# Kernel tuning notes

Measured on AMD Instinct MI355X. Metric: run time of the kernel, lower is better.

## Reference

```python
import jax, jax.numpy as jnp
import numpy as np

N_NODES = 50000
N_EDGES = 800000
D = 64
B = 64
HL = 128  # lstm hidden
OUT = 32


def setup_inputs() -> dict:
    key = jax.random.key(0)
    ks = jax.random.split(key, 16)
    s = 0.05
    return {
        "x": jax.random.normal(ks[0], (N_NODES, D), jnp.float32),
        "edge_index": jax.random.randint(ks[1], (2, N_EDGES), 0, N_NODES),
        "batch": jnp.sort(jax.random.randint(ks[2], (N_NODES,), 0, B)),
        "w1": jax.random.normal(ks[3], (D, D), jnp.float32) * s,
        "b1": jnp.zeros((D,), jnp.float32),
        "w2": jax.random.normal(ks[4], (D, D), jnp.float32) * s,
        "b2": jnp.zeros((D,), jnp.float32),
        "w3": jax.random.normal(ks[5], (D, D), jnp.float32) * s,
        "b3": jnp.zeros((D,), jnp.float32),
        "w4": jax.random.normal(ks[6], (D, D), jnp.float32) * s,
        "b4": jnp.zeros((D,), jnp.float32),
        "w_ih": jax.random.normal(ks[7], (4 * HL, D), jnp.float32) * s,
        "w_hh": jax.random.normal(ks[8], (4 * HL, HL), jnp.float32) * s,
        "b_ih": jnp.zeros((4 * HL,), jnp.float32),
        "b_hh": jnp.zeros((4 * HL,), jnp.float32),
        "fc_w": jax.random.normal(ks[9], (OUT, HL), jnp.float32) * s,
        "fc_b": jnp.zeros((OUT,), jnp.float32),
        "h0": jax.random.normal(ks[10], (1, B, HL), jnp.float32),
        "c0": jax.random.normal(ks[11], (1, B, HL), jnp.float32),
    }


def _gin(x, edge_index, wA, bA, wB, bB):
    # GINConv with eps=0: MLP(x + sum_{j->i} x_j); scatter-add over edges
    agg = jax.ops.segment_sum(x[edge_index[0]], edge_index[1], num_segments=N_NODES)
    h = x + agg
    h = jax.nn.relu(h @ wA.T + bA)
    return h @ wB.T + bB


def reference(x, edge_index, batch, w1, b1, w2, b2, w3, b3, w4, b4,
              w_ih, w_hh, b_ih, b_hh, fc_w, fc_b, h0, c0):
    h = jax.nn.relu(_gin(x, edge_index, w1, b1, w2, b2))  # dropout = identity (eval)
    h = jax.nn.relu(_gin(h, edge_index, w3, b3, w4, b4))
    # global_mean_pool over graphs
    sums = jax.ops.segment_sum(h, batch, num_segments=B)              # [B, D]
    cnts = jax.ops.segment_sum(jnp.ones((N_NODES,), h.dtype), batch, num_segments=B)
    pooled = sums / jnp.maximum(cnts, 1.0)[:, None]
    # single-step LSTM (PyTorch gate order: i, f, g, o)
    gates = pooled @ w_ih.T + b_ih + h0[0] @ w_hh.T + b_hh            # [B, 4H]
    i, f, g, o = jnp.split(gates, 4, axis=-1)
    c1 = jax.nn.sigmoid(f) * c0[0] + jax.nn.sigmoid(i) * jnp.tanh(g)
    h1 = jax.nn.sigmoid(o) * jnp.tanh(c1)
    logits = h1 @ fc_w.T + fc_b
    probs = jax.nn.softmax(logits, axis=1)
    return probs, h1[None], c1[None]
```

## Files before the change

### kernel.cpp

```cpp
#include <hip/hip_runtime.h>
#include <hip/hip_bf16.h>

#define N_NODES 50000
#define N_EDGES 800000
#define D 64
#define B 64
#define HL 128
#define OUT 32

#define CAP 64
#define STP 72
#define ZROW N_NODES

#define BINS 196
#define EPB 2048
#define LCAP 48
#define BCAP 4608

#define AB 391
#define CB 3125
#define MB 782

typedef __attribute__((ext_vector_type(8))) short          short8;
typedef __attribute__((ext_vector_type(8))) unsigned short ushort8_t;
typedef __attribute__((ext_vector_type(4))) float          floatx4;

__device__ __forceinline__ unsigned short f2bf(float f)
{
    unsigned u = __float_as_uint(f);
    u = (u + 0x7FFFu + ((u >> 16) & 1u)) >> 16;
    return (unsigned short)u;
}
__device__ __forceinline__ float bf2f(unsigned short s)
{
    return __uint_as_float(((unsigned)s) << 16);
}
__device__ __forceinline__ float bfLO(unsigned u) { return __uint_as_float(u << 16); }
__device__ __forceinline__ float bfHI(unsigned u) { return __uint_as_float(u & 0xffff0000u); }

__global__ __launch_bounds__(256) void fused_pro_kernel(
    const int*   __restrict__ ei,
    int*         __restrict__ bincnt,
    unsigned*    __restrict__ binbuf,
    const float* __restrict__ x, unsigned short* __restrict__ xb,
    const float* __restrict__ w1, const float* __restrict__ w2,
    const float* __restrict__ w3, const float* __restrict__ w4,
    unsigned short* __restrict__ wb,
    unsigned short* __restrict__ h1,
    float*       __restrict__ psum)
{
    __shared__ int      lcnt[BINS];
    __shared__ int      gbase[BINS];
    __shared__ unsigned lbuf[BINS * LCAP];

    int t = threadIdx.x;

    if (blockIdx.x < AB) {
        if (t < BINS) lcnt[t] = 0;
        __syncthreads();

        int base = blockIdx.x * EPB;
#pragma unroll
        for (int i = 0; i < EPB / 256; ++i) {
            int e = base + i * 256 + t;
            if (e < N_EDGES) {
                int s = ei[e];
                int d = ei[N_EDGES + e];
                int bin = d >> 8;
                unsigned pk = (unsigned)s | ((unsigned)(d & 255) << 16);
                int p = atomicAdd(&lcnt[bin], 1);
                if (p < LCAP) {
                    lbuf[bin * LCAP + p] = pk;
                } else {
                    int q = atomicAdd(&bincnt[bin], 1);
                    if (q < BCAP) binbuf[bin * BCAP + q] = pk;
                }
            }
        }
        __syncthreads();

        if (t < BINS) {
            int m = lcnt[t]; m = (m < LCAP) ? m : LCAP;
            gbase[t] = (m > 0) ? atomicAdd(&bincnt[t], m) : 0;
        }
        __syncthreads();

        int wv = t >> 6, lane = t & 63;
        for (int b = wv; b < BINS; b += 4) {
            int m = lcnt[b]; m = (m < LCAP) ? m : LCAP;
            int gb = gbase[b];
            for (int j = lane; j < m; j += 64)
                if (gb + j < BCAP) binbuf[b * BCAP + gb + j] = lbuf[b * LCAP + j];
        }
    } else if (blockIdx.x < AB + CB) {
        int cb = blockIdx.x - AB;
        int i = cb * 256 + t;
        const float4 v = reinterpret_cast<const float4*>(x)[i];
        ushort4 o;
        o.x = f2bf(v.x); o.y = f2bf(v.y); o.z = f2bf(v.z); o.w = f2bf(v.w);
        reinterpret_cast<ushort4*>(xb)[i] = o;

        if (cb < 64) {
            int j = cb * 256 + t;
            int m = j >> 12, off = j & 4095;
            const float* src = (m == 0) ? w1 : (m == 1) ? w2 : (m == 2) ? w3 : w4;
            wb[j] = f2bf(src[off]);
        }
    } else {
        if (t < D) {
            xb[(size_t)ZROW * D + t] = 0;
            h1[(size_t)ZROW * D + t] = 0;
        }
#pragma unroll
        for (int k = 0; k < 16; ++k)
            psum[t * 16 + k] = 0.0f;
    }
}

__device__ __forceinline__ void build_bucket64(
    const int*      __restrict__ bincnt,
    const unsigned* __restrict__ binbuf,
    unsigned short* lbkt,
    int*            lc,
    int bn0, int t)
{
    {
        ushort8_t fill = {ZROW, ZROW, ZROW, ZROW, ZROW, ZROW, ZROW, ZROW};
        reinterpret_cast<ushort8_t*>(lbkt)[t]       = fill;
        reinterpret_cast<ushort8_t*>(lbkt)[t + 256] = fill;
    }
    if (t < 64) lc[t] = 0;
    __syncthreads();

    const int bin = bn0 >> 8;
    const int q   = (bn0 >> 6) & 3;
    int m = bincnt[bin]; m = (m < BCAP) ? m : BCAP;
    const unsigned* src = binbuf + bin * BCAP;
    for (int j = t; j < m; j += 256) {
        unsigned pk = src[j];
        int dlow = (pk >> 16) & 255;
        if ((dlow >> 6) == q) {
            int r = dlow & 63;
            int p = atomicAdd(&lc[r], 1);
            if (p < CAP) lbkt[r * CAP + p] = (unsigned short)(pk & 0xFFFFu);
        }
    }
    __syncthreads();
}

__device__ __forceinline__ void gather16_lds(
    const unsigned short* __restrict__ feat,
    const unsigned short* lbkt,
    const int*            lc,
    unsigned short*       stw,
    int bn0, int wv, int lane)
{
    const int g = lane >> 4;
    const int c = lane & 15;

#pragma unroll
    for (int b = 0; b < 4; ++b) {
        const int rloc = wv * 16 + b * 4 + g;
        const int node = bn0 + rloc;
        int deg = lc[rloc];
        deg = (deg < CAP) ? deg : CAP;
        int m = (deg + 7) >> 3;
        {
            int t1 = __shfl_xor(m, 16); m = (t1 > m) ? t1 : m;
            int t2 = __shfl_xor(m, 32); m = (t2 > m) ? t2 : m;
        }

        const unsigned short* bkt = lbkt + rloc * CAP;

        uint2 u = *reinterpret_cast<const uint2*>(feat + (size_t)node * D + 4 * c);
        float a0 = bfLO(u.x), a1 = bfHI(u.x);
        float a2 = bfLO(u.y), a3 = bfHI(u.y);

        ushort8_t idx = *reinterpret_cast<const ushort8_t*>(bkt);
        for (int r = 0; r < m; ++r) {
            ushort8_t nxt = *reinterpret_cast<const ushort8_t*>(bkt + (r + 1) * 8);
#pragma unroll
            for (int j = 0; j < 8; ++j) {
                uint2 v = *reinterpret_cast<const uint2*>(
                    feat + (size_t)idx[j] * D + 4 * c);
                a0 += bfLO(v.x); a1 += bfHI(v.x);
                a2 += bfLO(v.y); a3 += bfHI(v.y);
            }
            idx = nxt;
        }

        uint2 o;
        o.x = (unsigned)f2bf(a0) | ((unsigned)f2bf(a1) << 16);
        o.y = (unsigned)f2bf(a2) | ((unsigned)f2bf(a3) << 16);
        *reinterpret_cast<uint2*>(stw + (b * 4 + g) * STP + 4 * c) = o;
    }
}

__global__ __launch_bounds__(256) void gmlp_kernel(
    const unsigned short* __restrict__ feat,
    const int*            __restrict__ bincnt,
    const unsigned*       __restrict__ binbuf,
    const unsigned short* __restrict__ wAb,
    const float*          __restrict__ bA,
    const unsigned short* __restrict__ wBb,
    const float*          __restrict__ bB,
    unsigned short*       __restrict__ outp)
{
    __shared__ int lc[64];
    __shared__ __align__(16) unsigned short lbkt[64 * CAP + 16];
    __shared__ __align__(16) unsigned short st[4][16 * STP];

    const int t    = threadIdx.x;
    const int wv   = t >> 6;
    const int lane = t & 63;
    const int quad = lane >> 4;
    const int col  = lane & 15;

    const int bn0 = blockIdx.x * 64;
    const int n0  = bn0 + wv * 16;

    build_bucket64(bincnt, binbuf, lbkt, lc, bn0, t);

    if (n0 >= N_NODES) return;

    float bAl[4], bBl[4];
#pragma unroll
    for (int tt = 0; tt < 4; ++tt) {
        bAl[tt] = bA[tt * 16 + col];
        bBl[tt] = bB[tt * 16 + col];
    }

    short8 WA[4][2], WB[4][2];
#pragma unroll
    for (int tt = 0; tt < 4; ++tt)
#pragma unroll
        for (int k = 0; k < 2; ++k) {
            WA[tt][k] = *reinterpret_cast<const short8*>(
                wAb + (tt * 16 + col) * D + k * 32 + quad * 8);
            WB[tt][k] = *reinterpret_cast<const short8*>(
                wBb + (tt * 16 + col) * D + k * 32 + quad * 8);
        }

    unsigned short* stw = &st[wv][0];

    gather16_lds(feat, lbkt, lc, stw, bn0, wv, lane);

    short8 A0 = *reinterpret_cast<const short8*>(stw + col * STP + 0 * 32 + quad * 8);
    short8 A1 = *reinterpret_cast<const short8*>(stw + col * STP + 1 * 32 + quad * 8);

#pragma unroll
    for (int tt = 0; tt < 4; ++tt) {
        floatx4 c = {0.0f, 0.0f, 0.0f, 0.0f};
        c = __builtin_amdgcn_mfma_f32_16x16x32_bf16(A0, WA[tt][0], c, 0, 0, 0);
        c = __builtin_amdgcn_mfma_f32_16x16x32_bf16(A1, WA[tt][1], c, 0, 0, 0);
#pragma unroll
        for (int r = 0; r < 4; ++r) {
            float v = fmaxf(c[r] + bAl[tt], 0.0f);
            stw[(quad * 4 + r) * STP + tt * 16 + col] = f2bf(v);
        }
    }

    short8 T0 = *reinterpret_cast<const short8*>(stw + col * STP + 0 * 32 + quad * 8);
    short8 T1 = *reinterpret_cast<const short8*>(stw + col * STP + 1 * 32 + quad * 8);

#pragma unroll
    for (int tt = 0; tt < 4; ++tt) {
        floatx4 c = {0.0f, 0.0f, 0.0f, 0.0f};
        c = __builtin_amdgcn_mfma_f32_16x16x32_bf16(T0, WB[tt][0], c, 0, 0, 0);
        c = __builtin_amdgcn_mfma_f32_16x16x32_bf16(T1, WB[tt][1], c, 0, 0, 0);
#pragma unroll
        for (int r = 0; r < 4; ++r) {
            float v = fmaxf(c[r] + bBl[tt], 0.0f);
            outp[(size_t)(n0 + quad * 4 + r) * D + tt * 16 + col] = f2bf(v);
        }
    }
}

__global__ __launch_bounds__(256) void g2mlp_pool_kernel(
    const unsigned short* __restrict__ feat,
    const int*            __restrict__ bincnt,
    const unsigned*       __restrict__ binbuf,
    const unsigned short* __restrict__ wAb,
    const float*          __restrict__ bA,
    const unsigned short* __restrict__ wBb,
    const float*          __restrict__ bB,
    const int*            __restrict__ batch,
    float*                __restrict__ psum)
{
    __shared__ int lc[64];
    __shared__ __align__(16) unsigned short lbkt[64 * CAP + 16];
    __shared__ __align__(16) unsigned short st[4][16 * STP];
    __shared__ float pt[64][D + 1];
    __shared__ int   sbatch[64];

    const int t    = threadIdx.x;
    const int wv   = t >> 6;
    const int lane = t & 63;
    const int quad = lane >> 4;
    const int col  = lane & 15;

    const int bn0 = blockIdx.x * 64;
    const int n0  = bn0 + wv * 16;
    const bool active = (n0 < N_NODES);

    if (t < 64) {
        int n = bn0 + t;
        sbatch[t] = (n < N_NODES) ? batch[n] : -1;
    }

    build_bucket64(bincnt, binbuf, lbkt, lc, bn0, t);

    if (active) {
        float bAl[4], bBl[4];
#pragma unroll
        for (int tt = 0; tt < 4; ++tt) {
            bAl[tt] = bA[tt * 16 + col];
            bBl[tt] = bB[tt * 16 + col];
        }

        short8 WA[4][2], WB[4][2];
#pragma unroll
        for (int tt = 0; tt < 4; ++tt)
#pragma unroll
            for (int k = 0; k < 2; ++k) {
                WA[tt][k] = *reinterpret_cast<const short8*>(
                    wAb + (tt * 16 + col) * D + k * 32 + quad * 8);
                WB[tt][k] = *reinterpret_cast<const short8*>(
                    wBb + (tt * 16 + col) * D + k * 32 + quad * 8);
            }

        unsigned short* stw = &st[wv][0];

        gather16_lds(feat, lbkt, lc, stw, bn0, wv, lane);

        short8 A0 = *reinterpret_cast<const short8*>(stw + col * STP + 0 * 32 + quad * 8);
        short8 A1 = *reinterpret_cast<const short8*>(stw + col * STP + 1 * 32 + quad * 8);

#pragma unroll
        for (int tt = 0; tt < 4; ++tt) {
            floatx4 c = {0.0f, 0.0f, 0.0f, 0.0f};
            c = __builtin_amdgcn_mfma_f32_16x16x32_bf16(A0, WA[tt][0], c, 0, 0, 0);
            c = __builtin_amdgcn_mfma_f32_16x16x32_bf16(A1, WA[tt][1], c, 0, 0, 0);
#pragma unroll
            for (int r = 0; r < 4; ++r) {
                float v = fmaxf(c[r] + bAl[tt], 0.0f);
                stw[(quad * 4 + r) * STP + tt * 16 + col] = f2bf(v);
            }
        }

        short8 T0 = *reinterpret_cast<const short8*>(stw + col * STP + 0 * 32 + quad * 8);
        short8 T1 = *reinterpret_cast<const short8*>(stw + col * STP + 1 * 32 + quad * 8);

#pragma unroll
        for (int tt = 0; tt < 4; ++tt) {
            floatx4 c = {0.0f, 0.0f, 0.0f, 0.0f};
            c = __builtin_amdgcn_mfma_f32_16x16x32_bf16(T0, WB[tt][0], c, 0, 0, 0);
            c = __builtin_amdgcn_mfma_f32_16x16x32_bf16(T1, WB[tt][1], c, 0, 0, 0);
#pragma unroll
            for (int r = 0; r < 4; ++r) {
                float v = fmaxf(c[r] + bBl[tt], 0.0f);
                pt[wv * 16 + quad * 4 + r][tt * 16 + col] = v;
            }
        }
    } else {
        for (int c2 = 0; c2 < 4; ++c2)
#pragma unroll
            for (int r = 0; r < 4; ++r)
                pt[wv * 16 + quad * 4 + r][c2 * 16 + col] = 0.0f;
    }
    __syncthreads();

    int q = t >> 6;
    int d = t & 63;
    float acc = 0.0f;
    int curg = sbatch[q * 16];
#pragma unroll
    for (int r = 0; r < 16; ++r) {
        int row = q * 16 + r;
        int g2 = sbatch[row];
        float v = pt[row][d];
        if (g2 != curg) {
            if (curg >= 0) atomicAdd(&psum[curg * D + d], acc);
            acc = 0.0f;
            curg = g2;
        }
        acc += v;
    }
    if (curg >= 0) atomicAdd(&psum[curg * D + d], acc);
}

__device__ __forceinline__ int lower_bound_dev(const int* a, int n, int v)
{
    int lo = 0, hi = n;
    while (lo < hi) {
        int m = (lo + hi) >> 1;
        if (a[m] < v) lo = m + 1; else hi = m;
    }
    return lo;
}

__device__ __forceinline__ float sigmoidf_(float x) { return 1.0f / (1.0f + expf(-x)); }

__global__ __launch_bounds__(512) void head_kernel(
    const float* __restrict__ psum,
    const int*   __restrict__ batch,
    const float* __restrict__ w_ih,
    const float* __restrict__ w_hh,
    const float* __restrict__ b_ih,
    const float* __restrict__ b_hh,
    const float* __restrict__ fc_w,
    const float* __restrict__ fc_b,
    const float* __restrict__ h0,
    const float* __restrict__ c0,
    float*       __restrict__ out_probs,
    float*       __restrict__ out_h1,
    float*       __restrict__ out_c1)
{
    int b = blockIdx.x;
    int j = threadIdx.x;

    __shared__ float sp[D];
    __shared__ float sh[HL];
    __shared__ float gates[4 * HL];
    __shared__ float sh1[HL];
    __shared__ float slog[OUT];

    if (j < D) {
        int start = lower_bound_dev(batch, N_NODES, b);
        int end   = lower_bound_dev(batch, N_NODES, b + 1);
        sp[j] = psum[b * D + j] / fmaxf((float)(end - start), 1.0f);
    } else if (j < D + HL) {
        sh[j - D] = h0[b * HL + (j - D)];
    }
    __syncthreads();

    {
        float acc = b_ih[j] + b_hh[j];
#pragma unroll
        for (int k = 0; k < D; ++k)  acc = fmaf(sp[k], w_ih[j * D + k], acc);
#pragma unroll
        for (int k = 0; k < HL; ++k) acc = fmaf(sh[k], w_hh[j * HL + k], acc);
        gates[j] = acc;
    }
    __syncthreads();

    if (j < HL) {
        float ig = gates[j];
        float fg = gates[HL + j];
        float gg = gates[2 * HL + j];
        float og = gates[3 * HL + j];
        float c  = sigmoidf_(fg) * c0[b * HL + j] + sigmoidf_(ig) * tanhf(gg);
        float hv = sigmoidf_(og) * tanhf(c);
        out_c1[b * HL + j] = c;
        out_h1[b * HL + j] = hv;
        sh1[j] = hv;
    }
    __syncthreads();

    if (j < OUT) {
        float a = fc_b[j];
#pragma unroll
        for (int k = 0; k < HL; ++k) a = fmaf(sh1[k], fc_w[j * HL + k], a);
        slog[j] = a;
    }
    __syncthreads();

    if (j < OUT) {
        float m = -1e30f;
#pragma unroll
        for (int k = 0; k < OUT; ++k) m = fmaxf(m, slog[k]);
        float s = 0.0f;
#pragma unroll
        for (int k = 0; k < OUT; ++k) s += expf(slog[k] - m);
        out_probs[b * OUT + j] = expf(slog[j] - m) / s;
    }
}

extern "C" void kernel_launch(void* const* d_in, const int* in_sizes, int n_in,
                              void* d_out, int out_size, void* d_ws, size_t ws_size,
                              hipStream_t stream)
{
    const float* x     = (const float*)d_in[0];
    const int*   ei    = (const int*)  d_in[1];
    const int*   batch = (const int*)  d_in[2];
    const float* w1    = (const float*)d_in[3];
    const float* b1    = (const float*)d_in[4];
    const float* w2    = (const float*)d_in[5];
    const float* b2    = (const float*)d_in[6];
    const float* w3    = (const float*)d_in[7];
    const float* b3    = (const float*)d_in[8];
    const float* w4    = (const float*)d_in[9];
    const float* b4    = (const float*)d_in[10];
    const float* w_ih  = (const float*)d_in[11];
    const float* w_hh  = (const float*)d_in[12];
    const float* b_ih  = (const float*)d_in[13];
    const float* b_hh  = (const float*)d_in[14];
    const float* fc_w  = (const float*)d_in[15];
    const float* fc_b  = (const float*)d_in[16];
    const float* h0    = (const float*)d_in[17];
    const float* c0    = (const float*)d_in[18];

    const size_t NR = (size_t)N_NODES + 16;
    int* bincnt = (int*)d_ws;
    unsigned* binbuf = (unsigned*)(bincnt + 256);
    unsigned short* xb = (unsigned short*)(binbuf + (size_t)BINS * BCAP);
    unsigned short* h1 = xb + NR * D;
    unsigned short* wb = h1 + NR * D;
    float* psum = (float*)(wb + 4 * D * D);

    float* out_probs = (float*)d_out;
    float* out_h1    = out_probs + B * OUT;
    float* out_c1    = out_h1 + B * HL;

    hipMemsetAsync(bincnt, 0, 256 * sizeof(int), stream);
    fused_pro_kernel<<<AB + CB + 1, 256, 0, stream>>>(
        ei, bincnt, binbuf, x, xb, w1, w2, w3, w4, wb, h1, psum);

    gmlp_kernel<<<MB, 256, 0, stream>>>(xb, bincnt, binbuf,
                                        wb, b1, wb + 4096, b2, h1);

    g2mlp_pool_kernel<<<MB, 256, 0, stream>>>(h1, bincnt, binbuf,
                                              wb + 8192, b3, wb + 12288, b4,
                                              batch, psum);

    head_kernel<<<B, 512, 0, stream>>>(psum, batch, w_ih, w_hh, b_ih, b_hh,
                                       fc_w, fc_b, h0, c0,
                                       out_probs, out_h1, out_c1);
}
```

Baseline: 199.0 us.

## Batch neighbor gathers across rows, double edges per bin block, fuse pool counts

The neighbor gather now walks all four rows of a wave together. It loads 32 feature vectors per step, which raises memory-level parallelism, at the cost of a shared trip count based on the largest degree and more registers. The edge binning blocks now handle twice as many edges each, so there are fewer blocks and more edges land in each block's local buffer. Per-graph node counts are gathered with atomics in the pooling kernel, replacing the binary searches over the batch array in the head kernel.

```diff
diff --git a/kernel.cpp b/kernel.cpp
--- a/kernel.cpp
+++ b/kernel.cpp
@@ -13,11 +13,11 @@
 #define ZROW N_NODES
 
 #define BINS 196
-#define EPB 2048
+#define EPB 4096
 #define LCAP 48
 #define BCAP 4608
 
-#define AB 391
+#define AB 196
 #define CB 3125
 #define MB 782
 
@@ -31,14 +31,10 @@
     u = (u + 0x7FFFu + ((u >> 16) & 1u)) >> 16;
     return (unsigned short)u;
 }
-__device__ __forceinline__ float bf2f(unsigned short s)
-{
-    return __uint_as_float(((unsigned)s) << 16);
-}
 __device__ __forceinline__ float bfLO(unsigned u) { return __uint_as_float(u << 16); }
 __device__ __forceinline__ float bfHI(unsigned u) { return __uint_as_float(u & 0xffff0000u); }
 
-__global__ __launch_bounds__(256) void fused_pro_kernel(
+__global__ __launch_bounds__(256) void pro_kernel(
     const int*   __restrict__ ei,
     int*         __restrict__ bincnt,
     unsigned*    __restrict__ binbuf,
@@ -47,7 +43,8 @@
     const float* __restrict__ w3, const float* __restrict__ w4,
     unsigned short* __restrict__ wb,
     unsigned short* __restrict__ h1,
-    float*       __restrict__ psum)
+    float*       __restrict__ psum,
+    float*       __restrict__ cnts)
 {
     __shared__ int      lcnt[BINS];
     __shared__ int      gbase[BINS];
@@ -60,7 +57,7 @@
         __syncthreads();
 
         int base = blockIdx.x * EPB;
-#pragma unroll
+#pragma unroll 8
         for (int i = 0; i < EPB / 256; ++i) {
             int e = base + i * 256 + t;
             if (e < N_EDGES) {
@@ -114,6 +111,7 @@
 #pragma unroll
         for (int k = 0; k < 16; ++k)
             psum[t * 16 + k] = 0.0f;
+        if (t < B) cnts[t] = 0.0f;
     }
 }
 
@@ -148,7 +146,7 @@
     __syncthreads();
 }
 
-__device__ __forceinline__ void gather16_lds(
+__device__ __forceinline__ void gather16_bf16(
     const unsigned short* __restrict__ feat,
     const unsigned short* lbkt,
     const int*            lc,
@@ -158,40 +156,57 @@
     const int g = lane >> 4;
     const int c = lane & 15;
 
+    int dmax = 0;
 #pragma unroll
     for (int b = 0; b < 4; ++b) {
-        const int rloc = wv * 16 + b * 4 + g;
-        const int node = bn0 + rloc;
-        int deg = lc[rloc];
-        deg = (deg < CAP) ? deg : CAP;
-        int m = (deg + 7) >> 3;
-        {
-            int t1 = __shfl_xor(m, 16); m = (t1 > m) ? t1 : m;
-            int t2 = __shfl_xor(m, 32); m = (t2 > m) ? t2 : m;
-        }
-
-        const unsigned short* bkt = lbkt + rloc * CAP;
-
+        int d = lc[wv * 16 + b * 4 + g];
+        d = (d < CAP) ? d : CAP;
+        dmax = (d > dmax) ? d : dmax;
+    }
+    int m = (dmax + 7) >> 3;
+    {
+        int t1 = __shfl_xor(m, 16); m = (t1 > m) ? t1 : m;
+        int t2 = __shfl_xor(m, 32); m = (t2 > m) ? t2 : m;
+    }
+
+    float a[4][4];
+#pragma unroll
+    for (int b = 0; b < 4; ++b) {
+        const int node = bn0 + wv * 16 + b * 4 + g;
         uint2 u = *reinterpret_cast<const uint2*>(feat + (size_t)node * D + 4 * c);
-        float a0 = bfLO(u.x), a1 = bfHI(u.x);
-        float a2 = bfLO(u.y), a3 = bfHI(u.y);
-
-        ushort8_t idx = *reinterpret_cast<const ushort8_t*>(bkt);
-        for (int r = 0; r < m; ++r) {
-            ushort8_t nxt = *reinterpret_cast<const ushort8_t*>(bkt + (r + 1) * 8);
+        a[b][0] = bfLO(u.x); a[b][1] = bfHI(u.x);
+        a[b][2] = bfLO(u.y); a[b][3] = bfHI(u.y);
+    }
+
+    for (int r = 0; r < m; ++r) {
+        ushort8_t idx[4];
+#pragma unroll
+        for (int b = 0; b < 4; ++b)
+            idx[b] = *reinterpret_cast<const ushort8_t*>(
+                lbkt + (wv * 16 + b * 4 + g) * CAP + r * 8);
+
+        uint2 v[4][8];
+#pragma unroll
+        for (int b = 0; b < 4; ++b)
+#pragma unroll
+            for (int j = 0; j < 8; ++j)
+                v[b][j] = *reinterpret_cast<const uint2*>(
+                    feat + (size_t)idx[b][j] * D + 4 * c);
+
+#pragma unroll
+        for (int b = 0; b < 4; ++b)
 #pragma unroll
             for (int j = 0; j < 8; ++j) {
-                uint2 v = *reinterpret_cast<const uint2*>(
-                    feat + (size_t)idx[j] * D + 4 * c);
-                a0 += bfLO(v.x); a1 += bfHI(v.x);
-                a2 += bfLO(v.y); a3 += bfHI(v.y);
+                a[b][0] += bfLO(v[b][j].x); a[b][1] += bfHI(v[b][j].x);
+                a[b][2] += bfLO(v[b][j].y); a[b][3] += bfHI(v[b][j].y);
             }
-            idx = nxt;
-        }
-
+    }
+
+#pragma unroll
+    for (int b = 0; b < 4; ++b) {
         uint2 o;
-        o.x = (unsigned)f2bf(a0) | ((unsigned)f2bf(a1) << 16);
-        o.y = (unsigned)f2bf(a2) | ((unsigned)f2bf(a3) << 16);
+        o.x = (unsigned)f2bf(a[b][0]) | ((unsigned)f2bf(a[b][1]) << 16);
+        o.y = (unsigned)f2bf(a[b][2]) | ((unsigned)f2bf(a[b][3]) << 16);
         *reinterpret_cast<uint2*>(stw + (b * 4 + g) * STP + 4 * c) = o;
     }
 }
@@ -243,7 +258,7 @@
 
     unsigned short* stw = &st[wv][0];
 
-    gather16_lds(feat, lbkt, lc, stw, bn0, wv, lane);
+    gather16_bf16(feat, lbkt, lc, stw, bn0, wv, lane);
 
     short8 A0 = *reinterpret_cast<const short8*>(stw + col * STP + 0 * 32 + quad * 8);
     short8 A1 = *reinterpret_cast<const short8*>(stw + col * STP + 1 * 32 + quad * 8);
@@ -285,7 +300,8 @@
     const unsigned short* __restrict__ wBb,
     const float*          __restrict__ bB,
     const int*            __restrict__ batch,
-    float*                __restrict__ psum)
+    float*                __restrict__ psum,
+    float*                __restrict__ cnts)
 {
     __shared__ int lc[64];
     __shared__ __align__(16) unsigned short lbkt[64 * CAP + 16];
@@ -331,7 +347,7 @@
 
         unsigned short* stw = &st[wv][0];
 
-        gather16_lds(feat, lbkt, lc, stw, bn0, wv, lane);
+        gather16_bf16(feat, lbkt, lc, stw, bn0, wv, lane);
 
         short8 A0 = *reinterpret_cast<const short8*>(stw + col * STP + 0 * 32 + quad * 8);
         short8 A1 = *reinterpret_cast<const short8*>(stw + col * STP + 1 * 32 + quad * 8);
@@ -373,6 +389,7 @@
     int q = t >> 6;
     int d = t & 63;
     float acc = 0.0f;
+    int   len = 0;
     int curg = sbatch[q * 16];
 #pragma unroll
     for (int r = 0; r < 16; ++r) {
@@ -380,30 +397,27 @@
         int g2 = sbatch[row];
         float v = pt[row][d];
         if (g2 != curg) {
-            if (curg >= 0) atomicAdd(&psum[curg * D + d], acc);
-            acc = 0.0f;
+            if (curg >= 0) {
+                atomicAdd(&psum[curg * D + d], acc);
+                if (d == 0) atomicAdd(&cnts[curg], (float)len);
+            }
+            acc = 0.0f; len = 0;
             curg = g2;
         }
         acc += v;
-    }
-    if (curg >= 0) atomicAdd(&psum[curg * D + d], acc);
-}
-
-__device__ __forceinline__ int lower_bound_dev(const int* a, int n, int v)
-{
-    int lo = 0, hi = n;
-    while (lo < hi) {
-        int m = (lo + hi) >> 1;
-        if (a[m] < v) lo = m + 1; else hi = m;
-    }
-    return lo;
+        len += 1;
+    }
+    if (curg >= 0) {
+        atomicAdd(&psum[curg * D + d], acc);
+        if (d == 0) atomicAdd(&cnts[curg], (float)len);
+    }
 }
 
 __device__ __forceinline__ float sigmoidf_(float x) { return 1.0f / (1.0f + expf(-x)); }
 
 __global__ __launch_bounds__(512) void head_kernel(
     const float* __restrict__ psum,
-    const int*   __restrict__ batch,
+    const float* __restrict__ cnts,
     const float* __restrict__ w_ih,
     const float* __restrict__ w_hh,
     const float* __restrict__ b_ih,
@@ -426,9 +440,7 @@
     __shared__ float slog[OUT];
 
     if (j < D) {
-        int start = lower_bound_dev(batch, N_NODES, b);
-        int end   = lower_bound_dev(batch, N_NODES, b + 1);
-        sp[j] = psum[b * D + j] / fmaxf((float)(end - start), 1.0f);
+        sp[j] = psum[b * D + j] / fmaxf(cnts[b], 1.0f);
     } else if (j < D + HL) {
         sh[j - D] = h0[b * HL + (j - D)];
     }
@@ -507,23 +519,24 @@
     unsigned short* h1 = xb + NR * D;
     unsigned short* wb = h1 + NR * D;
     float* psum = (float*)(wb + 4 * D * D);
+    float* cnts = psum + B * D;
 
     float* out_probs = (float*)d_out;
     float* out_h1    = out_probs + B * OUT;
     float* out_c1    = out_h1 + B * HL;
 
     hipMemsetAsync(bincnt, 0, 256 * sizeof(int), stream);
-    fused_pro_kernel<<<AB + CB + 1, 256, 0, stream>>>(
-        ei, bincnt, binbuf, x, xb, w1, w2, w3, w4, wb, h1, psum);
+    pro_kernel<<<AB + CB + 1, 256, 0, stream>>>(
+        ei, bincnt, binbuf, x, xb, w1, w2, w3, w4, wb, h1, psum, cnts);
 
     gmlp_kernel<<<MB, 256, 0, stream>>>(xb, bincnt, binbuf,
                                         wb, b1, wb + 4096, b2, h1);
 
     g2mlp_pool_kernel<<<MB, 256, 0, stream>>>(h1, bincnt, binbuf,
                                               wb + 8192, b3, wb + 12288, b4,
-                                              batch, psum);
-
-    head_kernel<<<B, 512, 0, stream>>>(psum, batch, w_ih, w_hh, b_ih, b_hh,
+                                              batch, psum, cnts);
+
+    head_kernel<<<B, 512, 0, stream>>>(psum, cnts, w_ih, w_hh, b_ih, b_hh,
                                        fc_w, fc_b, h0, c0,
                                        out_probs, out_h1, out_c1);
 }
```

Result: slower. 215.5 us (+8.3%).
